# Kernel optimization log

Hardware: AMD Instinct MI355X
Metric: run time of the kernel (lower is better)

## Reference

```python
import jax, jax.numpy as jnp
import numpy as np

N_GRAPHS = 500
EPS = 1e-5


def setup_inputs() -> dict:
    key = jax.random.key(0)
    ks = jax.random.split(key, 10)
    N, H, OUT, E = 50000, 96, 10, 800000
    s = 1.0 / np.sqrt(H)
    x = jax.random.normal(ks[0], (N, H), jnp.float32)
    edge_index = jax.random.randint(ks[1], (2, E), 0, N, jnp.int32)
    batch = jnp.sort(jax.random.randint(ks[2], (N,), 0, N_GRAPHS, jnp.int32))
    convW = jax.random.normal(ks[3], (6, H, H), jnp.float32) * s
    convB = jnp.zeros((6, H), jnp.float32)
    bnG = jnp.ones((5, H), jnp.float32)
    bnB = jnp.zeros((5, H), jnp.float32)
    W1 = jax.random.normal(ks[4], (H, H), jnp.float32) * s
    b1 = jnp.zeros((H,), jnp.float32)
    g1 = jnp.ones((H,), jnp.float32)
    be1 = jnp.zeros((H,), jnp.float32)
    W2 = jax.random.normal(ks[5], (H, H), jnp.float32) * s
    b2 = jnp.zeros((H,), jnp.float32)
    W3 = jax.random.normal(ks[6], (H, OUT), jnp.float32) * s
    b3 = jnp.zeros((OUT,), jnp.float32)
    return dict(x=x, edge_index=edge_index, batch=batch, convW=convW, convB=convB,
                bnG=bnG, bnB=bnB, W1=W1, b1=b1, g1=g1, be1=be1, W2=W2, b2=b2, W3=W3, b3=b3)


def _batchnorm(h, g, b):
    # track_running_stats=False -> always use batch statistics (biased var)
    mu = h.mean(axis=0)
    v = jnp.mean((h - mu) ** 2, axis=0)
    return (h - mu) * jax.lax.rsqrt(v + EPS) * g + b


def reference(x, edge_index, batch, convW, convB, bnG, bnB, W1, b1, g1, be1, W2, b2, W3, b3):
    N = x.shape[0]
    src, dst = edge_index[0], edge_index[1]
    # GCN symmetric normalization with self-loops: A_hat = D^-1/2 (A+I) D^-1/2
    deg = jnp.zeros((N,), x.dtype).at[dst].add(1.0) + 1.0  # +1 for self loop
    dinv = jax.lax.rsqrt(deg)
    ew = dinv[src] * dinv[dst]            # [E] edge weights
    self_w = dinv * dinv                   # [N] self-loop weights (1/deg)

    def gcn_conv(h, W, b):
        h = h @ W
        agg = jnp.zeros_like(h).at[dst].add(ew[:, None] * h[src])
        return agg + self_w[:, None] * h + b

    # PyG BasicGNN: layers 0..4 -> conv+norm+relu+dropout; layer 5 -> conv only.
    # Dropout is identity in eval mode.
    for i in range(6):
        x = gcn_conv(x, convW[i], convB[i])
        if i < 5:
            x = jax.nn.relu(_batchnorm(x, bnG[i], bnB[i]))

    # global_mean_pool over `batch`
    cnt = jax.ops.segment_sum(jnp.ones((N,), x.dtype), batch, num_segments=N_GRAPHS)
    pooled = jax.ops.segment_sum(x, batch, num_segments=N_GRAPHS) / jnp.maximum(cnt, 1.0)[:, None]

    # prediction head: Linear -> BN -> ReLU -> (Dropout) -> Linear -> ReLU -> Linear
    h = jax.nn.relu(_batchnorm(pooled @ W1 + b1, g1, be1))
    h = jax.nn.relu(h @ W2 + b2)
    return h @ W3 + b3
```

## Files before the change

### kernel.cpp

```cpp
#include <hip/hip_runtime.h>
#include <hip/hip_fp16.h>

#define HF 96
#define C4 24
#define CH 12
#define NGRAPHS 500
#define EPS 1e-5f

__device__ __forceinline__ float4 h4tof4(uint2 u) {
    __half2 a = *(__half2*)&u.x;
    __half2 b = *(__half2*)&u.y;
    float2 fa = __half22float2(a);
    float2 fb = __half22float2(b);
    return make_float4(fa.x, fa.y, fb.x, fb.y);
}


__global__ void count_kernel(const int* __restrict__ dst, int E, int* __restrict__ cnt) {
    int stride = gridDim.x * blockDim.x;
    for (int i = blockIdx.x * blockDim.x + threadIdx.x; i < E; i += stride)
        atomicAdd(&cnt[dst[i]], 1);
}

__global__ void node_init_kernel(const int* __restrict__ cnt, int N,
                                 float* __restrict__ dinv, float* __restrict__ selfw) {
    int stride = gridDim.x * blockDim.x;
    for (int i = blockIdx.x * blockDim.x + threadIdx.x; i < N; i += stride) {
        float d = (float)(cnt[i] + 1);
        dinv[i] = 1.0f / sqrtf(d);
        selfw[i] = 1.0f / d;
    }
}

__global__ void scan1_kernel(const int* __restrict__ cnt, int N, int* __restrict__ bsum) {
    __shared__ int s[256];
    int t = threadIdx.x;
    int i = blockIdx.x * 256 + t;
    s[t] = (i < N) ? cnt[i] : 0;
    __syncthreads();
    for (int off = 128; off; off >>= 1) {
        if (t < off) s[t] += s[t + off];
        __syncthreads();
    }
    if (t == 0) bsum[blockIdx.x] = s[0];
}

__global__ void scan2_kernel(const int* __restrict__ bsum, int NB,
                             int* __restrict__ boff, int* __restrict__ row_ptr, int N) {
    __shared__ int s[256];
    int t = threadIdx.x;
    int v = (t < NB) ? bsum[t] : 0;
    s[t] = v;
    __syncthreads();
    for (int off = 1; off < 256; off <<= 1) {
        int u = (t >= off) ? s[t - off] : 0;
        __syncthreads();
        s[t] += u;
        __syncthreads();
    }
    if (t < NB) boff[t] = s[t] - v;
    if (t == 255) row_ptr[N] = s[255];
}

__global__ void scan3_kernel(int* __restrict__ cnt, int N, const int* __restrict__ boff,
                             int* __restrict__ row_ptr) {
    __shared__ int s[256];
    int t = threadIdx.x;
    int i = blockIdx.x * 256 + t;
    int v = (i < N) ? cnt[i] : 0;
    s[t] = v;
    __syncthreads();
    for (int off = 1; off < 256; off <<= 1) {
        int u = (t >= off) ? s[t - off] : 0;
        __syncthreads();
        s[t] += u;
        __syncthreads();
    }
    if (i < N) {
        row_ptr[i] = boff[blockIdx.x] + s[t] - v;
        cnt[i] = 0;
    }
}

__global__ void scatter_kernel(const int* __restrict__ src, const int* __restrict__ dst, int E,
                               const int* __restrict__ row_ptr, int* __restrict__ cnt,
                               const float* __restrict__ dinv,
                               int2* __restrict__ csr) {
    int stride = gridDim.x * blockDim.x;
    for (int i = blockIdx.x * blockDim.x + threadIdx.x; i < E; i += stride) {
        int d = dst[i], s = src[i];
        int p = row_ptr[d] + atomicAdd(&cnt[d], 1);
        float w = dinv[s] * dinv[d];
        csr[p] = make_int2(s, __float_as_int(w));
    }
}


__global__ __launch_bounds__(256) void
matmul_kernel(const float* __restrict__ in, const float* __restrict__ W,
              __half* __restrict__ out, int N, int applyBN,
              const double* __restrict__ bnsum,
              const float* __restrict__ bnG, const float* __restrict__ bnB) {
    __shared__ float4 sW[HF * C4];
    __shared__ float4 sAl[C4], sBe[C4];
    for (int i = threadIdx.x; i < HF * C4; i += blockDim.x)
        sW[i] = ((const float4*)W)[i];
    if (threadIdx.x < HF) {
        float a = 1.f, b = 0.f;
        if (applyBN) {
            double invN = 1.0 / (double)N;
            double mu = bnsum[threadIdx.x] * invN;
            double var = bnsum[HF + threadIdx.x] * invN - mu * mu;
            float v = fmaxf((float)var, 0.f) + EPS;
            a = bnG[threadIdx.x] / sqrtf(v);
            b = bnB[threadIdx.x] - (float)mu * a;
        }
        ((float*)sAl)[threadIdx.x] = a;
        ((float*)sBe)[threadIdx.x] = b;
    }
    __syncthreads();
    int nG = (N + 3) >> 2;
    int total = nG * C4;
    int stride = gridDim.x * blockDim.x;
    for (int idx = blockIdx.x * blockDim.x + threadIdx.x; idx < total; idx += stride) {
        int ng = idx / C4, c = idx % C4;
        int n0 = ng * 4;
        int rem = N - n0;
        const float4* r0 = (const float4*)(in + (size_t)n0 * HF);
        const float4* r1 = r0 + ((rem > 1) ? C4 : 0);
        const float4* r2 = r0 + ((rem > 2) ? 2 * C4 : 0);
        const float4* r3 = r0 + ((rem > 3) ? 3 * C4 : 0);
        float4 acc0 = make_float4(0.f, 0.f, 0.f, 0.f);
        float4 acc1 = acc0, acc2 = acc0, acc3 = acc0;
#pragma unroll 4
        for (int k4 = 0; k4 < C4; ++k4) {
            float4 al = sAl[k4], be = sBe[k4];
            float4 w0 = sW[(k4 * 4 + 0) * C4 + c];
            float4 w1 = sW[(k4 * 4 + 1) * C4 + c];
            float4 w2 = sW[(k4 * 4 + 2) * C4 + c];
            float4 w3 = sW[(k4 * 4 + 3) * C4 + c];
            float4 a0 = r0[k4], a1 = r1[k4], a2 = r2[k4], a3 = r3[k4];
            if (applyBN) {
                a0.x = fmaxf(fmaf(a0.x, al.x, be.x), 0.f); a0.y = fmaxf(fmaf(a0.y, al.y, be.y), 0.f);
                a0.z = fmaxf(fmaf(a0.z, al.z, be.z), 0.f); a0.w = fmaxf(fmaf(a0.w, al.w, be.w), 0.f);
                a1.x = fmaxf(fmaf(a1.x, al.x, be.x), 0.f); a1.y = fmaxf(fmaf(a1.y, al.y, be.y), 0.f);
                a1.z = fmaxf(fmaf(a1.z, al.z, be.z), 0.f); a1.w = fmaxf(fmaf(a1.w, al.w, be.w), 0.f);
                a2.x = fmaxf(fmaf(a2.x, al.x, be.x), 0.f); a2.y = fmaxf(fmaf(a2.y, al.y, be.y), 0.f);
                a2.z = fmaxf(fmaf(a2.z, al.z, be.z), 0.f); a2.w = fmaxf(fmaf(a2.w, al.w, be.w), 0.f);
                a3.x = fmaxf(fmaf(a3.x, al.x, be.x), 0.f); a3.y = fmaxf(fmaf(a3.y, al.y, be.y), 0.f);
                a3.z = fmaxf(fmaf(a3.z, al.z, be.z), 0.f); a3.w = fmaxf(fmaf(a3.w, al.w, be.w), 0.f);
            }
#define ACC(ACCV, AV) \
            ACCV.x = fmaf(AV.x, w0.x, fmaf(AV.y, w1.x, fmaf(AV.z, w2.x, fmaf(AV.w, w3.x, ACCV.x)))); \
            ACCV.y = fmaf(AV.x, w0.y, fmaf(AV.y, w1.y, fmaf(AV.z, w2.y, fmaf(AV.w, w3.y, ACCV.y)))); \
            ACCV.z = fmaf(AV.x, w0.z, fmaf(AV.y, w1.z, fmaf(AV.z, w2.z, fmaf(AV.w, w3.z, ACCV.z)))); \
            ACCV.w = fmaf(AV.x, w0.w, fmaf(AV.y, w1.w, fmaf(AV.z, w2.w, fmaf(AV.w, w3.w, ACCV.w))));
            ACC(acc0, a0) ACC(acc1, a1) ACC(acc2, a2) ACC(acc3, a3)
#undef ACC
        }
        uint2* orow = (uint2*)out;
#define STORE(J, ACCV) \
        if (rem > J) { \
            __half2 lo = __floats2half2_rn(ACCV.x, ACCV.y); \
            __half2 hi = __floats2half2_rn(ACCV.z, ACCV.w); \
            orow[(size_t)(n0 + J) * C4 + c] = make_uint2(*(unsigned int*)&lo, *(unsigned int*)&hi); \
        }
        STORE(0, acc0) STORE(1, acc1) STORE(2, acc2) STORE(3, acc3)
#undef STORE
    }
}


__global__ __launch_bounds__(256) void
agg_kernel(const __half* __restrict__ Hb, float* __restrict__ out,
           const int* __restrict__ row_ptr, const int2* __restrict__ csr,
           const float* __restrict__ selfw, const float* __restrict__ convB,
           int N, double* __restrict__ bnsum) {
    __shared__ float sred[2 * HF];
    bool stats = (bnsum != nullptr);
    for (int i = threadIdx.x; i < 2 * HF; i += blockDim.x) sred[i] = 0.f;
    __syncthreads();
    const uint4* h4p = (const uint4*)Hb;
    int total = N * CH;
    int stride = gridDim.x * blockDim.x;
    for (int idx = blockIdx.x * blockDim.x + threadIdx.x; idx < total; idx += stride) {
        int n = idx / CH, c = idx % CH;
        const uint4* hp = h4p + c;
        int p0 = row_ptr[n], p1 = row_ptr[n + 1];
        float sw = selfw[n];
        uint4 hraw = hp[(size_t)n * CH];
        float4 hlo = h4tof4(make_uint2(hraw.x, hraw.y));
        float4 hhi = h4tof4(make_uint2(hraw.z, hraw.w));
        float4 blo = ((const float4*)convB)[2 * c];
        float4 bhi = ((const float4*)convB)[2 * c + 1];
        float4 alo, ahi;
        alo.x = fmaf(sw, hlo.x, blo.x); alo.y = fmaf(sw, hlo.y, blo.y);
        alo.z = fmaf(sw, hlo.z, blo.z); alo.w = fmaf(sw, hlo.w, blo.w);
        ahi.x = fmaf(sw, hhi.x, bhi.x); ahi.y = fmaf(sw, hhi.y, bhi.y);
        ahi.z = fmaf(sw, hhi.z, bhi.z); ahi.w = fmaf(sw, hhi.w, bhi.w);
#define EDGE(EV, RV) { \
            float w = __int_as_float(EV.y); \
            float4 vlo = h4tof4(make_uint2(RV.x, RV.y)); \
            float4 vhi = h4tof4(make_uint2(RV.z, RV.w)); \
            alo.x = fmaf(w, vlo.x, alo.x); alo.y = fmaf(w, vlo.y, alo.y); \
            alo.z = fmaf(w, vlo.z, alo.z); alo.w = fmaf(w, vlo.w, alo.w); \
            ahi.x = fmaf(w, vhi.x, ahi.x); ahi.y = fmaf(w, vhi.y, ahi.y); \
            ahi.z = fmaf(w, vhi.z, ahi.z); ahi.w = fmaf(w, vhi.w, ahi.w); }
        int p = p0;
        for (; p + 8 <= p1; p += 8) {
            int2 e0 = csr[p + 0], e1 = csr[p + 1], e2 = csr[p + 2], e3 = csr[p + 3];
            int2 e4 = csr[p + 4], e5 = csr[p + 5], e6 = csr[p + 6], e7 = csr[p + 7];
            uint4 g0 = hp[(size_t)e0.x * CH];
            uint4 g1 = hp[(size_t)e1.x * CH];
            uint4 g2 = hp[(size_t)e2.x * CH];
            uint4 g3 = hp[(size_t)e3.x * CH];
            uint4 g4 = hp[(size_t)e4.x * CH];
            uint4 g5 = hp[(size_t)e5.x * CH];
            uint4 g6 = hp[(size_t)e6.x * CH];
            uint4 g7 = hp[(size_t)e7.x * CH];
            EDGE(e0, g0) EDGE(e1, g1) EDGE(e2, g2) EDGE(e3, g3)
            EDGE(e4, g4) EDGE(e5, g5) EDGE(e6, g6) EDGE(e7, g7)
        }
        for (; p + 4 <= p1; p += 4) {
            int2 e0 = csr[p + 0], e1 = csr[p + 1], e2 = csr[p + 2], e3 = csr[p + 3];
            uint4 g0 = hp[(size_t)e0.x * CH];
            uint4 g1 = hp[(size_t)e1.x * CH];
            uint4 g2 = hp[(size_t)e2.x * CH];
            uint4 g3 = hp[(size_t)e3.x * CH];
            EDGE(e0, g0) EDGE(e1, g1) EDGE(e2, g2) EDGE(e3, g3)
        }
        for (; p < p1; ++p) {
            int2 e = csr[p];
            uint4 g = hp[(size_t)e.x * CH];
            EDGE(e, g)
        }
#undef EDGE
        ((float4*)out)[2 * idx]     = alo;
        ((float4*)out)[2 * idx + 1] = ahi;
        if (stats) {
            int f = 8 * c;
            atomicAdd(&sred[f + 0], alo.x); atomicAdd(&sred[f + 1], alo.y);
            atomicAdd(&sred[f + 2], alo.z); atomicAdd(&sred[f + 3], alo.w);
            atomicAdd(&sred[f + 4], ahi.x); atomicAdd(&sred[f + 5], ahi.y);
            atomicAdd(&sred[f + 6], ahi.z); atomicAdd(&sred[f + 7], ahi.w);
            atomicAdd(&sred[HF + f + 0], alo.x * alo.x); atomicAdd(&sred[HF + f + 1], alo.y * alo.y);
            atomicAdd(&sred[HF + f + 2], alo.z * alo.z); atomicAdd(&sred[HF + f + 3], alo.w * alo.w);
            atomicAdd(&sred[HF + f + 4], ahi.x * ahi.x); atomicAdd(&sred[HF + f + 5], ahi.y * ahi.y);
            atomicAdd(&sred[HF + f + 6], ahi.z * ahi.z); atomicAdd(&sred[HF + f + 7], ahi.w * ahi.w);
        }
    }
    if (stats) {
        __syncthreads();
        for (int i = threadIdx.x; i < 2 * HF; i += blockDim.x)
            atomicAdd(&bnsum[i], (double)sred[i]);
    }
}


__global__ __launch_bounds__(128) void
pool_head1_kernel(const float* __restrict__ xin, const int* __restrict__ batch, int N,
                  const float* __restrict__ W1, const float* __restrict__ b1,
                  float* __restrict__ tmp1, double* __restrict__ bnsum) {
    __shared__ float row[HF];
    int g = blockIdx.x;
    int lo = 0, hi = N;
    while (lo < hi) { int m = (lo + hi) >> 1; if (batch[m] < g) lo = m + 1; else hi = m; }
    int s0 = lo;
    lo = s0; hi = N;
    while (lo < hi) { int m = (lo + hi) >> 1; if (batch[m] < g + 1) lo = m + 1; else hi = m; }
    int s1 = lo;
    int f = threadIdx.x;
    if (f < HF) {
        float sum = 0.f;
        for (int n = s0; n < s1; ++n) sum += xin[(size_t)n * HF + f];
        float inv = 1.0f / fmaxf((float)(s1 - s0), 1.0f);
        row[f] = sum * inv;
    }
    __syncthreads();
    if (f < HF) {
        float acc = b1[f];
        for (int k = 0; k < HF; ++k) acc = fmaf(row[k], W1[k * HF + f], acc);
        tmp1[g * HF + f] = acc;
        atomicAdd(&bnsum[f], (double)acc);
        atomicAdd(&bnsum[HF + f], (double)(acc * acc));
    }
}

__global__ __launch_bounds__(128) void
head23_kernel(const float* __restrict__ tmp1, const double* __restrict__ bnsum,
              const float* __restrict__ g1, const float* __restrict__ be1,
              const float* __restrict__ W2, const float* __restrict__ b2,
              const float* __restrict__ W3, const float* __restrict__ b3,
              float* __restrict__ out) {
    __shared__ float row[HF], row2[HF];
    int g = blockIdx.x;
    int f = threadIdx.x;
    if (f < HF) {
        double mu = bnsum[f] / (double)NGRAPHS;
        double var = bnsum[HF + f] / (double)NGRAPHS - mu * mu;
        float v = fmaxf((float)var, 0.f) + EPS;
        float a = g1[f] / sqrtf(v);
        float bb = be1[f] - (float)mu * a;
        row[f] = fmaxf(fmaf(tmp1[g * HF + f], a, bb), 0.f);
    }
    __syncthreads();
    if (f < HF) {
        float acc = b2[f];
        for (int k = 0; k < HF; ++k) acc = fmaf(row[k], W2[k * HF + f], acc);
        row2[f] = fmaxf(acc, 0.f);
    }
    __syncthreads();
    if (f < 10) {
        float acc = b3[f];
        for (int k = 0; k < HF; ++k) acc = fmaf(row2[k], W3[k * 10 + f], acc);
        out[g * 10 + f] = acc;
    }
}


extern "C" void kernel_launch(void* const* d_in, const int* in_sizes, int n_in,
                              void* d_out, int out_size, void* d_ws, size_t ws_size,
                              hipStream_t stream) {
    (void)n_in; (void)out_size; (void)ws_size;
    const float* x     = (const float*)d_in[0];
    const int*   ei    = (const int*)d_in[1];
    const int*   batch = (const int*)d_in[2];
    const float* convW = (const float*)d_in[3];
    const float* convB = (const float*)d_in[4];
    const float* bnG   = (const float*)d_in[5];
    const float* bnB   = (const float*)d_in[6];
    const float* W1    = (const float*)d_in[7];
    const float* b1    = (const float*)d_in[8];
    const float* g1    = (const float*)d_in[9];
    const float* be1   = (const float*)d_in[10];
    const float* W2    = (const float*)d_in[11];
    const float* b2    = (const float*)d_in[12];
    const float* W3    = (const float*)d_in[13];
    const float* b3    = (const float*)d_in[14];
    float* outp = (float*)d_out;

    int N = in_sizes[0] / HF;
    int E = in_sizes[1] / 2;
    int NB = (N + 255) / 256;
    const int* src  = ei;
    const int* dstp = ei + E;

    char* ws = (char*)d_ws;
    size_t off = 0;
    auto alloc = [&](size_t bytes) -> char* {
        char* p = ws + off;
        off += (bytes + 255) & ~(size_t)255;
        return p;
    };
    __half* Hb     = (__half*)alloc((size_t)N * HF * 2);
    float* Ob      = (float*)alloc((size_t)N * HF * 4);
    int2*  csr     = (int2*)alloc((size_t)E * 8);
    int*   row_ptr = (int*)alloc((size_t)(N + 1) * 4);
    float* dinv    = (float*)alloc((size_t)N * 4);
    float* selfw   = (float*)alloc((size_t)N * 4);
    int*   bsum    = (int*)alloc((size_t)NB * 4);
    int*   boff    = (int*)alloc((size_t)NB * 4);
    float* tmp1    = (float*)alloc((size_t)NGRAPHS * HF * 4);
    char* zstart   = ws + off;
    int*    cnt    = (int*)alloc((size_t)N * 4);
    double* bns    = (double*)alloc(6 * 2 * HF * 8);
    size_t zbytes  = (size_t)((ws + off) - zstart);

    hipMemsetAsync(zstart, 0, zbytes, stream);

    count_kernel<<<1024, 256, 0, stream>>>(dstp, E, cnt);
    node_init_kernel<<<(N + 255) / 256, 256, 0, stream>>>(cnt, N, dinv, selfw);
    scan1_kernel<<<NB, 256, 0, stream>>>(cnt, N, bsum);
    scan2_kernel<<<1, 256, 0, stream>>>(bsum, NB, boff, row_ptr, N);
    scan3_kernel<<<NB, 256, 0, stream>>>(cnt, N, boff, row_ptr);
    scatter_kernel<<<1024, 256, 0, stream>>>(src, dstp, E, row_ptr, cnt, dinv, csr);

    int agg_grid = (N * CH + 255) / 256;
    const float* cur = x;
    for (int i = 0; i < 6; ++i) {
        int nG = (N + 3) >> 2;
        int mm_grid = (nG * C4 + 255) / 256;
        matmul_kernel<<<mm_grid, 256, 0, stream>>>(
            cur, convW + (size_t)i * HF * HF, Hb, N,
            (i > 0) ? 1 : 0,
            (i > 0) ? bns + (size_t)(i - 1) * 2 * HF : nullptr,
            (i > 0) ? bnG + (size_t)(i - 1) * HF : nullptr,
            (i > 0) ? bnB + (size_t)(i - 1) * HF : nullptr);
        agg_kernel<<<agg_grid, 256, 0, stream>>>(
            Hb, Ob, row_ptr, csr, selfw,
            convB + (size_t)i * HF, N,
            (i < 5) ? bns + (size_t)i * 2 * HF : nullptr);
        cur = Ob;
    }

    pool_head1_kernel<<<NGRAPHS, 128, 0, stream>>>(Ob, batch, N, W1, b1, tmp1, bns + 5 * 2 * HF);
    head23_kernel<<<NGRAPHS, 128, 0, stream>>>(tmp1, bns + 5 * 2 * HF, g1, be1, W2, b2, W3, b3, outp);
}
```

Before: 854.1 us.

## Split each node's edge list across four lanes in GCN aggregation

```diff
diff --git a/kernel.cpp b/kernel.cpp
--- a/kernel.cpp
+++ b/kernel.cpp
@@ -171,7 +171,7 @@
 }
 
 
-__global__ __launch_bounds__(256) void
+__global__ __launch_bounds__(256, 4) void
 agg_kernel(const __half* __restrict__ Hb, float* __restrict__ out,
            const int* __restrict__ row_ptr, const int2* __restrict__ csr,
            const float* __restrict__ selfw, const float* __restrict__ convB,
@@ -181,23 +181,29 @@
     for (int i = threadIdx.x; i < 2 * HF; i += blockDim.x) sred[i] = 0.f;
     __syncthreads();
     const uint4* h4p = (const uint4*)Hb;
-    int total = N * CH;
+    int total = N * CH * 4;
     int stride = gridDim.x * blockDim.x;
     for (int idx = blockIdx.x * blockDim.x + threadIdx.x; idx < total; idx += stride) {
-        int n = idx / CH, c = idx % CH;
+        int n = idx / (CH * 4);
+        int r = idx % (CH * 4);
+        int c = r >> 2;
+        int s = r & 3;
         const uint4* hp = h4p + c;
         int p0 = row_ptr[n], p1 = row_ptr[n + 1];
-        float sw = selfw[n];
-        uint4 hraw = hp[(size_t)n * CH];
-        float4 hlo = h4tof4(make_uint2(hraw.x, hraw.y));
-        float4 hhi = h4tof4(make_uint2(hraw.z, hraw.w));
-        float4 blo = ((const float4*)convB)[2 * c];
-        float4 bhi = ((const float4*)convB)[2 * c + 1];
-        float4 alo, ahi;
-        alo.x = fmaf(sw, hlo.x, blo.x); alo.y = fmaf(sw, hlo.y, blo.y);
-        alo.z = fmaf(sw, hlo.z, blo.z); alo.w = fmaf(sw, hlo.w, blo.w);
-        ahi.x = fmaf(sw, hhi.x, bhi.x); ahi.y = fmaf(sw, hhi.y, bhi.y);
-        ahi.z = fmaf(sw, hhi.z, bhi.z); ahi.w = fmaf(sw, hhi.w, bhi.w);
+        float4 alo = make_float4(0.f, 0.f, 0.f, 0.f);
+        float4 ahi = alo;
+        if (s == 0) {
+            float sw = selfw[n];
+            uint4 hraw = hp[(size_t)n * CH];
+            float4 hlo = h4tof4(make_uint2(hraw.x, hraw.y));
+            float4 hhi = h4tof4(make_uint2(hraw.z, hraw.w));
+            float4 blo = ((const float4*)convB)[2 * c];
+            float4 bhi = ((const float4*)convB)[2 * c + 1];
+            alo.x = fmaf(sw, hlo.x, blo.x); alo.y = fmaf(sw, hlo.y, blo.y);
+            alo.z = fmaf(sw, hlo.z, blo.z); alo.w = fmaf(sw, hlo.w, blo.w);
+            ahi.x = fmaf(sw, hhi.x, bhi.x); ahi.y = fmaf(sw, hhi.y, bhi.y);
+            ahi.z = fmaf(sw, hhi.z, bhi.z); ahi.w = fmaf(sw, hhi.w, bhi.w);
+        }
 #define EDGE(EV, RV) { \
             float w = __int_as_float(EV.y); \
             float4 vlo = h4tof4(make_uint2(RV.x, RV.y)); \
@@ -206,47 +212,42 @@
             alo.z = fmaf(w, vlo.z, alo.z); alo.w = fmaf(w, vlo.w, alo.w); \
             ahi.x = fmaf(w, vhi.x, ahi.x); ahi.y = fmaf(w, vhi.y, ahi.y); \
             ahi.z = fmaf(w, vhi.z, ahi.z); ahi.w = fmaf(w, vhi.w, ahi.w); }
-        int p = p0;
-        for (; p + 8 <= p1; p += 8) {
-            int2 e0 = csr[p + 0], e1 = csr[p + 1], e2 = csr[p + 2], e3 = csr[p + 3];
-            int2 e4 = csr[p + 4], e5 = csr[p + 5], e6 = csr[p + 6], e7 = csr[p + 7];
-            uint4 g0 = hp[(size_t)e0.x * CH];
-            uint4 g1 = hp[(size_t)e1.x * CH];
-            uint4 g2 = hp[(size_t)e2.x * CH];
-            uint4 g3 = hp[(size_t)e3.x * CH];
-            uint4 g4 = hp[(size_t)e4.x * CH];
-            uint4 g5 = hp[(size_t)e5.x * CH];
-            uint4 g6 = hp[(size_t)e6.x * CH];
-            uint4 g7 = hp[(size_t)e7.x * CH];
-            EDGE(e0, g0) EDGE(e1, g1) EDGE(e2, g2) EDGE(e3, g3)
-            EDGE(e4, g4) EDGE(e5, g5) EDGE(e6, g6) EDGE(e7, g7)
-        }
-        for (; p + 4 <= p1; p += 4) {
-            int2 e0 = csr[p + 0], e1 = csr[p + 1], e2 = csr[p + 2], e3 = csr[p + 3];
+        int p = p0 + s;
+        for (; p + 12 < p1; p += 16) {
+            int2 e0 = csr[p], e1 = csr[p + 4], e2 = csr[p + 8], e3 = csr[p + 12];
             uint4 g0 = hp[(size_t)e0.x * CH];
             uint4 g1 = hp[(size_t)e1.x * CH];
             uint4 g2 = hp[(size_t)e2.x * CH];
             uint4 g3 = hp[(size_t)e3.x * CH];
             EDGE(e0, g0) EDGE(e1, g1) EDGE(e2, g2) EDGE(e3, g3)
         }
-        for (; p < p1; ++p) {
+        for (; p < p1; p += 4) {
             int2 e = csr[p];
             uint4 g = hp[(size_t)e.x * CH];
             EDGE(e, g)
         }
 #undef EDGE
-        ((float4*)out)[2 * idx]     = alo;
-        ((float4*)out)[2 * idx + 1] = ahi;
-        if (stats) {
-            int f = 8 * c;
-            atomicAdd(&sred[f + 0], alo.x); atomicAdd(&sred[f + 1], alo.y);
-            atomicAdd(&sred[f + 2], alo.z); atomicAdd(&sred[f + 3], alo.w);
-            atomicAdd(&sred[f + 4], ahi.x); atomicAdd(&sred[f + 5], ahi.y);
-            atomicAdd(&sred[f + 6], ahi.z); atomicAdd(&sred[f + 7], ahi.w);
-            atomicAdd(&sred[HF + f + 0], alo.x * alo.x); atomicAdd(&sred[HF + f + 1], alo.y * alo.y);
-            atomicAdd(&sred[HF + f + 2], alo.z * alo.z); atomicAdd(&sred[HF + f + 3], alo.w * alo.w);
-            atomicAdd(&sred[HF + f + 4], ahi.x * ahi.x); atomicAdd(&sred[HF + f + 5], ahi.y * ahi.y);
-            atomicAdd(&sred[HF + f + 6], ahi.z * ahi.z); atomicAdd(&sred[HF + f + 7], ahi.w * ahi.w);
+        for (int m = 1; m <= 2; m <<= 1) {
+            alo.x += __shfl_xor(alo.x, m); alo.y += __shfl_xor(alo.y, m);
+            alo.z += __shfl_xor(alo.z, m); alo.w += __shfl_xor(alo.w, m);
+            ahi.x += __shfl_xor(ahi.x, m); ahi.y += __shfl_xor(ahi.y, m);
+            ahi.z += __shfl_xor(ahi.z, m); ahi.w += __shfl_xor(ahi.w, m);
+        }
+        if (s == 0) {
+            int o = n * CH + c;
+            ((float4*)out)[2 * o]     = alo;
+            ((float4*)out)[2 * o + 1] = ahi;
+            if (stats) {
+                int f = 8 * c;
+                atomicAdd(&sred[f + 0], alo.x); atomicAdd(&sred[f + 1], alo.y);
+                atomicAdd(&sred[f + 2], alo.z); atomicAdd(&sred[f + 3], alo.w);
+                atomicAdd(&sred[f + 4], ahi.x); atomicAdd(&sred[f + 5], ahi.y);
+                atomicAdd(&sred[f + 6], ahi.z); atomicAdd(&sred[f + 7], ahi.w);
+                atomicAdd(&sred[HF + f + 0], alo.x * alo.x); atomicAdd(&sred[HF + f + 1], alo.y * alo.y);
+                atomicAdd(&sred[HF + f + 2], alo.z * alo.z); atomicAdd(&sred[HF + f + 3], alo.w * alo.w);
+                atomicAdd(&sred[HF + f + 4], ahi.x * ahi.x); atomicAdd(&sred[HF + f + 5], ahi.y * ahi.y);
+                atomicAdd(&sred[HF + f + 6], ahi.z * ahi.z); atomicAdd(&sred[HF + f + 7], ahi.w * ahi.w);
+            }
         }
     }
     if (stats) {
@@ -375,7 +376,7 @@
     scan3_kernel<<<NB, 256, 0, stream>>>(cnt, N, boff, row_ptr);
     scatter_kernel<<<1024, 256, 0, stream>>>(src, dstp, E, row_ptr, cnt, dinv, csr);
 
-    int agg_grid = (N * CH + 255) / 256;
+    int agg_grid = (N * CH * 4 + 255) / 256;
     const float* cur = x;
     for (int i = 0; i < 6; ++i) {
         int nG = (N + 3) >> 2;
```

After: 1.509 ms. 76.7% more time.

## Split aggregation into three feature-chunk passes with nontemporal index and output traffic

Applied to the files above, without the earlier changes.

```diff
diff --git a/kernel.cpp b/kernel.cpp
--- a/kernel.cpp
+++ b/kernel.cpp
@@ -4,6 +4,8 @@
 #define HF 96
 #define C4 24
 #define CH 12
+#define NPASS 3
+#define CPP 4
 #define NGRAPHS 500
 #define EPS 1e-5f
 
@@ -13,6 +15,17 @@
     float2 fa = __half22float2(a);
     float2 fb = __half22float2(b);
     return make_float4(fa.x, fa.y, fb.x, fb.y);
+}
+
+__device__ __forceinline__ int2 ld_nt_int2(const int2* p) {
+    typedef int i2 __attribute__((ext_vector_type(2)));
+    i2 v = __builtin_nontemporal_load((const i2*)p);
+    return make_int2(v.x, v.y);
+}
+__device__ __forceinline__ void st_nt_f4(float* p, float4 v) {
+    typedef float f4 __attribute__((ext_vector_type(4)));
+    f4 t; t.x = v.x; t.y = v.y; t.z = v.z; t.w = v.w;
+    __builtin_nontemporal_store(t, (f4*)p);
 }
 
 
@@ -172,22 +185,24 @@
 
 
 __global__ __launch_bounds__(256) void
-agg_kernel(const __half* __restrict__ Hb, float* __restrict__ out,
-           const int* __restrict__ row_ptr, const int2* __restrict__ csr,
-           const float* __restrict__ selfw, const float* __restrict__ convB,
-           int N, double* __restrict__ bnsum) {
+agg_pass_kernel(const __half* __restrict__ Hb, float* __restrict__ out,
+                const int* __restrict__ row_ptr, const int2* __restrict__ csr,
+                const float* __restrict__ selfw, const float* __restrict__ convB,
+                int N, int c0, double* __restrict__ bnsum) {
     __shared__ float sred[2 * HF];
     bool stats = (bnsum != nullptr);
     for (int i = threadIdx.x; i < 2 * HF; i += blockDim.x) sred[i] = 0.f;
     __syncthreads();
     const uint4* h4p = (const uint4*)Hb;
-    int total = N * CH;
+    int total = N * CPP;
     int stride = gridDim.x * blockDim.x;
     for (int idx = blockIdx.x * blockDim.x + threadIdx.x; idx < total; idx += stride) {
-        int n = idx / CH, c = idx % CH;
+        int n = idx >> 2;
+        int c = c0 + (idx & 3);
         const uint4* hp = h4p + c;
-        int p0 = row_ptr[n], p1 = row_ptr[n + 1];
-        float sw = selfw[n];
+        int p0 = __builtin_nontemporal_load(row_ptr + n);
+        int p1 = __builtin_nontemporal_load(row_ptr + n + 1);
+        float sw = __builtin_nontemporal_load(selfw + n);
         uint4 hraw = hp[(size_t)n * CH];
         float4 hlo = h4tof4(make_uint2(hraw.x, hraw.y));
         float4 hhi = h4tof4(make_uint2(hraw.z, hraw.w));
@@ -207,22 +222,11 @@
             ahi.x = fmaf(w, vhi.x, ahi.x); ahi.y = fmaf(w, vhi.y, ahi.y); \
             ahi.z = fmaf(w, vhi.z, ahi.z); ahi.w = fmaf(w, vhi.w, ahi.w); }
         int p = p0;
-        for (; p + 8 <= p1; p += 8) {
-            int2 e0 = csr[p + 0], e1 = csr[p + 1], e2 = csr[p + 2], e3 = csr[p + 3];
-            int2 e4 = csr[p + 4], e5 = csr[p + 5], e6 = csr[p + 6], e7 = csr[p + 7];
-            uint4 g0 = hp[(size_t)e0.x * CH];
-            uint4 g1 = hp[(size_t)e1.x * CH];
-            uint4 g2 = hp[(size_t)e2.x * CH];
-            uint4 g3 = hp[(size_t)e3.x * CH];
-            uint4 g4 = hp[(size_t)e4.x * CH];
-            uint4 g5 = hp[(size_t)e5.x * CH];
-            uint4 g6 = hp[(size_t)e6.x * CH];
-            uint4 g7 = hp[(size_t)e7.x * CH];
-            EDGE(e0, g0) EDGE(e1, g1) EDGE(e2, g2) EDGE(e3, g3)
-            EDGE(e4, g4) EDGE(e5, g5) EDGE(e6, g6) EDGE(e7, g7)
-        }
         for (; p + 4 <= p1; p += 4) {
-            int2 e0 = csr[p + 0], e1 = csr[p + 1], e2 = csr[p + 2], e3 = csr[p + 3];
+            int2 e0 = ld_nt_int2(csr + p);
+            int2 e1 = ld_nt_int2(csr + p + 1);
+            int2 e2 = ld_nt_int2(csr + p + 2);
+            int2 e3 = ld_nt_int2(csr + p + 3);
             uint4 g0 = hp[(size_t)e0.x * CH];
             uint4 g1 = hp[(size_t)e1.x * CH];
             uint4 g2 = hp[(size_t)e2.x * CH];
@@ -230,13 +234,14 @@
             EDGE(e0, g0) EDGE(e1, g1) EDGE(e2, g2) EDGE(e3, g3)
         }
         for (; p < p1; ++p) {
-            int2 e = csr[p];
+            int2 e = ld_nt_int2(csr + p);
             uint4 g = hp[(size_t)e.x * CH];
             EDGE(e, g)
         }
 #undef EDGE
-        ((float4*)out)[2 * idx]     = alo;
-        ((float4*)out)[2 * idx + 1] = ahi;
+        int o = n * CH + c;
+        st_nt_f4(out + 8 * (size_t)o, alo);
+        st_nt_f4(out + 8 * (size_t)o + 4, ahi);
         if (stats) {
             int f = 8 * c;
             atomicAdd(&sred[f + 0], alo.x); atomicAdd(&sred[f + 1], alo.y);
@@ -375,7 +380,7 @@
     scan3_kernel<<<NB, 256, 0, stream>>>(cnt, N, boff, row_ptr);
     scatter_kernel<<<1024, 256, 0, stream>>>(src, dstp, E, row_ptr, cnt, dinv, csr);
 
-    int agg_grid = (N * CH + 255) / 256;
+    int agg_grid = (N * CPP + 255) / 256;
     const float* cur = x;
     for (int i = 0; i < 6; ++i) {
         int nG = (N + 3) >> 2;
@@ -386,10 +391,12 @@
             (i > 0) ? bns + (size_t)(i - 1) * 2 * HF : nullptr,
             (i > 0) ? bnG + (size_t)(i - 1) * HF : nullptr,
             (i > 0) ? bnB + (size_t)(i - 1) * HF : nullptr);
-        agg_kernel<<<agg_grid, 256, 0, stream>>>(
-            Hb, Ob, row_ptr, csr, selfw,
-            convB + (size_t)i * HF, N,
-            (i < 5) ? bns + (size_t)i * 2 * HF : nullptr);
+        for (int pass = 0; pass < NPASS; ++pass) {
+            agg_pass_kernel<<<agg_grid, 256, 0, stream>>>(
+                Hb, Ob, row_ptr, csr, selfw,
+                convB + (size_t)i * HF, N, pass * CPP,
+                (i < 5) ? bns + (size_t)i * 2 * HF : nullptr);
+        }
         cur = Ob;
     }
 
```

New measurement: 1.077 ms. 26.1% more time.
